# Optimization experiments

Hardware: AMD Instinct MI355X
Metric: run time of the kernel (lower is better)

## Reference

```python
import jax, jax.numpy as jnp
import numpy as np

B, CIN, COUT, K, STRIDE, PAD = 32, 64, 128, 3, 1, 1
IN_H, IN_W = 112, 112


def setup_inputs() -> dict:
    key = jax.random.key(0)
    k1, k2 = jax.random.split(key)
    # x_padded already has `PAD` rows/cols of zeros on each side, as in the torch module
    x = jax.random.normal(k1, (B, CIN, IN_H, IN_W), dtype=jnp.float32)
    x_padded = jnp.pad(x, ((0, 0), (0, 0), (PAD, PAD), (PAD, PAD)))
    weight = jax.random.normal(k2, (COUT, CIN, K, K), dtype=jnp.float32) * 0.1
    bias = jnp.zeros((COUT,), dtype=jnp.float32)
    return {
        "x_padded": x_padded,
        "in_height": IN_H,
        "in_width": IN_W,
        "weight": weight,
        "bias": bias,
    }


def reference(x_padded, in_height, in_width, weight, bias):
    # CustomConv2D.custom_conv2d: direct conv over the pre-padded input.
    # out[b,o,h,w] = sum_{i,kh,kw} x_padded[b,i,h*s+kh,w*s+kw] * weight[o,i,kh,kw] + bias[o]
    out = jax.lax.conv_general_dilated(
        x_padded, weight,
        window_strides=(STRIDE, STRIDE),
        padding="VALID",  # padding already applied to x_padded
        dimension_numbers=("NCHW", "OIHW", "NCHW"),
    )
    return out + bias[None, :, None, None]
```

## Files before the change

### kernel.cpp

```cpp
#include <hip/hip_runtime.h>

typedef __attribute__((ext_vector_type(8))) short short8;
typedef __attribute__((ext_vector_type(4))) float f32x4;
typedef __attribute__((ext_vector_type(4))) unsigned int u32x4;
typedef unsigned short u16;
typedef unsigned int u32;
typedef unsigned long long u64;

#define XH 114
#define XW 114
#define CINC 64
#define COUT 128
#define OH 112
#define OW 112
#define NB 32
#define KTOT 576

static __device__ __forceinline__ u16 f2bf(float f) {
    u32 x = __float_as_uint(f);
    u32 r = (x + 0x7fffu + ((x >> 16) & 1u)) >> 16;
    return (u16)r;
}

#define MFMA16(a, b, c) __builtin_amdgcn_mfma_f32_16x16x32_bf16((a), (b), (c), 0, 0, 0)

static __device__ __forceinline__ void gload16(const void* g, void* l) {
    __builtin_amdgcn_global_load_lds(
        (const __attribute__((address_space(1))) unsigned int*)g,
        (__attribute__((address_space(3))) unsigned int*)l, 16, 0, 0);
}


__global__ __launch_bounds__(256) void wcvt_reord(const float* __restrict__ w,
                                                  u16* __restrict__ wbf) {
    int i = blockIdx.x * 256 + threadIdx.x;
    int o = i / KTOT;
    int rem = i - o * KTOT;
    int khkw = rem >> 6;
    int ci = rem & 63;
    wbf[i] = f2bf(w[(o * CINC + ci) * 9 + khkw]);
}

__global__ __launch_bounds__(256) void xcvt(const float* __restrict__ x,
                                            u16* __restrict__ xb) {
    __shared__ u16 tile[XW * 70];
    const int blk = blockIdx.x;
    const int b = blk / XH;
    const int h = blk - b * XH;
    const int tid = threadIdx.x;

    #pragma unroll
    for (int it = 0; it < 15; ++it) {
        int idx = it * 256 + tid;
        if (idx < 32 * XW) {
            int cp = idx / XW;
            int w_ = idx - cp * XW;
            const float* s0 = x + ((size_t)(b * CINC + 2 * cp) * XH + h) * XW + w_;
            float a = s0[0];
            float c = s0[XH * XW];
            u32 pk = (u32)f2bf(a) | ((u32)f2bf(c) << 16);
            *(u32*)&tile[w_ * 70 + 2 * cp] = pk;
        }
    }
    __syncthreads();

    u16* dstrow = xb + (size_t)(b * XH + h) * (XW * CINC);
    #pragma unroll
    for (int p2 = 0; p2 < 4; ++p2) {
        int task = p2 * 256 + tid;
        if (task < XW * 8) {
            int w_ = task >> 3;
            int c8 = task & 7;
            const u32* s = (const u32*)&tile[w_ * 70 + c8 * 8];
            u32x4 v = {s[0], s[1], s[2], s[3]};
            int slot = c8 ^ ((2 * h + w_) & 7);
            *(u32x4*)(dstrow + w_ * CINC + slot * 8) = v;
        }
    }
}

__global__ __launch_bounds__(512, 4) void conv_r5(const u16* __restrict__ xb,
                                                  const u16* __restrict__ wbf,
                                                  const float* __restrict__ bias,
                                                  float* __restrict__ out) {
    __shared__ u16 ldsB[4 * XW * CINC];
    char* ldsc = (char*)ldsB;

    const int tid = threadIdx.x;
    int bid = blockIdx.x;
    {
        int xcd = bid & 7;
        bid = xcd * 224 + (bid >> 3);
    }
    const int b  = bid / 56;
    const int h0 = (bid - b * 56) * 2;

    const int lane = tid & 63;
    const int wv   = tid >> 6;

    {
        const char* src = (const char*)(xb + (size_t)(b * XH + h0) * (XW * CINC));
        #pragma unroll
        for (int it = 0; it < 8; ++it) {
            int off = it * 8192 + wv * 1024;
            if (off < 4 * XW * CINC * 2) {
                gload16(src + off + lane * 16, ldsc + off);
            }
        }
    }
    __syncthreads();

    const int l16  = lane & 15;
    const int lhi  = lane >> 4;
    const int wm   = wv & 3;
    const int wn   = wv >> 2;

    const u16* wrow0 = wbf + (wm * 32 + l16) * KTOT + lhi * 8;
    const u16* wrow1 = wrow0 + 16 * KTOT;

    f32x4 acc[2][7];
    const f32x4 zero = {0.f, 0.f, 0.f, 0.f};
    #pragma unroll
    for (int i = 0; i < 2; ++i)
        #pragma unroll
        for (int j = 0; j < 7; ++j) acc[i][j] = zero;

    short8 aA0 = *(const short8*)(wrow0);
    short8 aA1 = *(const short8*)(wrow1);
    short8 aB0, aB1;

    #pragma unroll 1
    for (int tt = 0; tt < 9; ++tt) {
        const int t0 = 2 * tt;
        aB0 = *(const short8*)(wrow0 + (t0 + 1) * 32);
        aB1 = *(const short8*)(wrow1 + (t0 + 1) * 32);

        const int kh = tt / 3;
        const int kw = tt - kh * 3;
        const int r  = wn + kh;
        const int pix0 = r * XW + kw + l16;
        const int hash = (2 * (h0 + r) + kw + l16) & 7;
        const int baddr0 = (pix0 << 7) + ((lhi ^ hash) << 4);

        {
            __builtin_amdgcn_s_setprio(1);
            #pragma unroll
            for (int nf = 0; nf < 7; ++nf) {
                short8 bf = *(const short8*)(ldsc + baddr0 + nf * 2048);
                acc[0][nf] = MFMA16(aA0, bf, acc[0][nf]);
                acc[1][nf] = MFMA16(aA1, bf, acc[1][nf]);
            }
            __builtin_amdgcn_s_setprio(0);
        }
        if (tt < 8) {
            aA0 = *(const short8*)(wrow0 + (t0 + 2) * 32);
            aA1 = *(const short8*)(wrow1 + (t0 + 2) * 32);
        }
        {
            __builtin_amdgcn_s_setprio(1);
            #pragma unroll
            for (int nf = 0; nf < 7; ++nf) {
                short8 bf = *(const short8*)(ldsc + (baddr0 ^ 0x40) + nf * 2048);
                acc[0][nf] = MFMA16(aB0, bf, acc[0][nf]);
                acc[1][nf] = MFMA16(aB1, bf, acc[1][nf]);
            }
            __builtin_amdgcn_s_setprio(0);
        }
    }

    float* outb = out + (size_t)b * COUT * (OH * OW) + (h0 + wn) * OW;
    #pragma unroll
    for (int mf = 0; mf < 2; ++mf) {
        #pragma unroll
        for (int j = 0; j < 4; ++j) {
            const int o = wm * 32 + mf * 16 + lhi * 4 + j;
            const float bv = bias[o];
            #pragma unroll
            for (int nf = 0; nf < 7; ++nf) {
                outb[(size_t)o * (OH * OW) + nf * 16 + l16] = acc[mf][nf][j] + bv;
            }
        }
    }
}


#define BK 32
#define NSTEP 18
#define LDB 40

__global__ __launch_bounds__(256) void wcvt_ident(const float* __restrict__ w,
                                                  u16* __restrict__ wbf) {
    int i = blockIdx.x * 256 + threadIdx.x;
    if (i < COUT * KTOT) wbf[i] = f2bf(w[i]);
}

__global__ __launch_bounds__(256) void conv_fb(const float* __restrict__ x,
                                               const u16* __restrict__ wbf,
                                               const float* __restrict__ bias,
                                               float* __restrict__ out) {
    __shared__ u16 ldsB[OW * LDB];
    const int tid = threadIdx.x;
    int bid = blockIdx.x;
    { int xcd = bid & 7; bid = xcd * 448 + (bid >> 3); }
    const int b = bid / OH;
    const int h = bid - b * OH;
    const float* xbp = x + (size_t)b * (CINC * XH * XW);
    float* outb = out + (size_t)b * (COUT * OH * OW) + h * OW;
    const int lane = tid & 63, wv = tid >> 6, l16 = lane & 15, lhi = lane >> 4;
    const int m0 = wv * 32;
    const int sk = tid >> 3, sn0 = (tid & 7) * 14;
    f32x4 acc[2][7];
    const f32x4 zero = {0.f, 0.f, 0.f, 0.f};
    #pragma unroll
    for (int i = 0; i < 2; ++i)
        #pragma unroll
        for (int j = 0; j < 7; ++j) acc[i][j] = zero;
    for (int t = 0; t < NSTEP; ++t) {
        const int kg = t * BK + sk;
        const int ci = kg / 9;
        const int r9 = kg - ci * 9;
        const int kh = r9 / 3, kw = r9 - (r9 / 3) * 3;
        const float* src = xbp + ((size_t)ci * XH + (h + kh)) * XW + kw + sn0;
        __syncthreads();
        #pragma unroll
        for (int i = 0; i < 14; ++i) ldsB[(sn0 + i) * LDB + sk] = f2bf(src[i]);
        __syncthreads();
        short8 afrag[2];
        #pragma unroll
        for (int mf = 0; mf < 2; ++mf)
            afrag[mf] = *(const short8*)(wbf + (m0 + mf * 16 + l16) * KTOT + t * BK + lhi * 8);
        #pragma unroll
        for (int nf = 0; nf < 7; ++nf) {
            short8 bfrag = *(const short8*)&ldsB[(nf * 16 + l16) * LDB + lhi * 8];
            acc[0][nf] = MFMA16(afrag[0], bfrag, acc[0][nf]);
            acc[1][nf] = MFMA16(afrag[1], bfrag, acc[1][nf]);
        }
    }
    #pragma unroll
    for (int mf = 0; mf < 2; ++mf)
        #pragma unroll
        for (int j = 0; j < 4; ++j) {
            const int o = m0 + mf * 16 + lhi * 4 + j;
            const float bv = bias[o];
            #pragma unroll
            for (int nf = 0; nf < 7; ++nf)
                outb[(size_t)o * (OH * OW) + nf * 16 + l16] = acc[mf][nf][j] + bv;
        }
}

extern "C" void kernel_launch(void* const* d_in, const int* in_sizes, int n_in,
                              void* d_out, int out_size, void* d_ws, size_t ws_size,
                              hipStream_t stream) {
    const float* x    = (const float*)d_in[0];
    const float* w    = (const float*)d_in[3];
    const float* bias = (const float*)d_in[4];
    float* out = (float*)d_out;

    const size_t WBYTES = (size_t)COUT * KTOT * 2;
    const size_t XBYTES = (size_t)NB * XH * XW * CINC * 2;
    if (ws_size >= WBYTES + XBYTES) {
        u16* wbf = (u16*)d_ws;
        u16* xb  = (u16*)((char*)d_ws + WBYTES);
        wcvt_reord<<<(COUT * KTOT) / 256, 256, 0, stream>>>(w, wbf);
        xcvt<<<NB * XH, 256, 0, stream>>>(x, xb);
        conv_r5<<<NB * 56, 512, 0, stream>>>(xb, wbf, bias, out);
    } else {
        u16* wbf = (u16*)d_ws;
        wcvt_ident<<<(COUT * KTOT + 255) / 256, 256, 0, stream>>>(w, wbf);
        conv_fb<<<NB * OH, 256, 0, stream>>>(x, wbf, bias, out);
    }
}
```

Baseline: 129.7 us.

## Make conv kernel persistent with double-buffered LDS tiles and register-resident weights

Result: faster. 122.1 us (-5.9%).

```diff
diff --git a/kernel.cpp b/kernel.cpp
--- a/kernel.cpp
+++ b/kernel.cpp
@@ -15,6 +15,7 @@
 #define OW 112
 #define NB 32
 #define KTOT 576
+#define TILEB 58368
 
 static __device__ __forceinline__ u16 f2bf(float f) {
     u32 x = __float_as_uint(f);
@@ -79,105 +80,108 @@
     }
 }
 
-__global__ __launch_bounds__(512, 4) void conv_r5(const u16* __restrict__ xb,
-                                                  const u16* __restrict__ wbf,
-                                                  const float* __restrict__ bias,
-                                                  float* __restrict__ out) {
-    __shared__ u16 ldsB[4 * XW * CINC];
-    char* ldsc = (char*)ldsB;
-
-    const int tid = threadIdx.x;
-    int bid = blockIdx.x;
-    {
-        int xcd = bid & 7;
-        bid = xcd * 224 + (bid >> 3);
-    }
-    const int b  = bid / 56;
-    const int h0 = (bid - b * 56) * 2;
-
+__global__ __launch_bounds__(512, 2) void conv_pers(const u16* __restrict__ xb,
+                                                    const u16* __restrict__ wbf,
+                                                    const float* __restrict__ bias,
+                                                    float* __restrict__ out) {
+    __shared__ u16 lds[2 * 4 * XW * CINC];
+    char* ldsc = (char*)lds;
+
+    const int tid  = threadIdx.x;
     const int lane = tid & 63;
     const int wv   = tid >> 6;
-
-    {
-        const char* src = (const char*)(xb + (size_t)(b * XH + h0) * (XW * CINC));
-        #pragma unroll
-        for (int it = 0; it < 8; ++it) {
-            int off = it * 8192 + wv * 1024;
-            if (off < 4 * XW * CINC * 2) {
-                gload16(src + off + lane * 16, ldsc + off);
-            }
-        }
-    }
-    __syncthreads();
-
     const int l16  = lane & 15;
     const int lhi  = lane >> 4;
     const int wm   = wv & 3;
     const int wn   = wv >> 2;
 
+    const int t0g = blockIdx.x * 7;
+
     const u16* wrow0 = wbf + (wm * 32 + l16) * KTOT + lhi * 8;
     const u16* wrow1 = wrow0 + 16 * KTOT;
-
-    f32x4 acc[2][7];
+    short8 areg[18][2];
+    #pragma unroll
+    for (int t = 0; t < 18; ++t) {
+        areg[t][0] = *(const short8*)(wrow0 + t * 32);
+        areg[t][1] = *(const short8*)(wrow1 + t * 32);
+    }
+
+    {
+        const char* src = (const char*)(xb + (size_t)((t0g / 56) * XH + (t0g % 56) * 2) * (XW * CINC));
+        #pragma unroll
+        for (int it = 0; it < 8; ++it) {
+            int off = it * 8192 + wv * 1024;
+            if (off < TILEB) gload16(src + off + lane * 16, ldsc + off);
+        }
+    }
+
     const f32x4 zero = {0.f, 0.f, 0.f, 0.f};
-    #pragma unroll
-    for (int i = 0; i < 2; ++i)
-        #pragma unroll
-        for (int j = 0; j < 7; ++j) acc[i][j] = zero;
-
-    short8 aA0 = *(const short8*)(wrow0);
-    short8 aA1 = *(const short8*)(wrow1);
-    short8 aB0, aB1;
 
     #pragma unroll 1
-    for (int tt = 0; tt < 9; ++tt) {
-        const int t0 = 2 * tt;
-        aB0 = *(const short8*)(wrow0 + (t0 + 1) * 32);
-        aB1 = *(const short8*)(wrow1 + (t0 + 1) * 32);
-
-        const int kh = tt / 3;
-        const int kw = tt - kh * 3;
-        const int r  = wn + kh;
-        const int pix0 = r * XW + kw + l16;
-        const int hash = (2 * (h0 + r) + kw + l16) & 7;
-        const int baddr0 = (pix0 << 7) + ((lhi ^ hash) << 4);
-
-        {
+    for (int i = 0; i < 7; ++i) {
+        __syncthreads();
+
+        if (i < 6) {
+            const int tg = t0g + i + 1;
+            const char* src = (const char*)(xb + (size_t)((tg / 56) * XH + (tg % 56) * 2) * (XW * CINC));
+            char* dstb = ldsc + ((i + 1) & 1) * TILEB;
+            #pragma unroll
+            for (int it = 0; it < 8; ++it) {
+                int off = it * 8192 + wv * 1024;
+                if (off < TILEB) gload16(src + off + lane * 16, dstb + off);
+            }
+        }
+
+        const int tg = t0g + i;
+        const int b  = tg / 56;
+        const int h0 = (tg - b * 56) * 2;
+        char* buf = ldsc + (i & 1) * TILEB;
+
+        f32x4 acc[2][7];
+        #pragma unroll
+        for (int mf = 0; mf < 2; ++mf)
+            #pragma unroll
+            for (int nf = 0; nf < 7; ++nf) acc[mf][nf] = zero;
+
+        #pragma unroll
+        for (int tt = 0; tt < 9; ++tt) {
+            const int kh = tt / 3;
+            const int kw = tt - kh * 3;
+            const int r  = wn + kh;
+            const int pix0 = r * XW + kw + l16;
+            const int hash = (2 * (h0 + r) + kw + l16) & 7;
+            const int ba0 = (pix0 << 7) + ((lhi ^ hash) << 4);
+
             __builtin_amdgcn_s_setprio(1);
             #pragma unroll
             for (int nf = 0; nf < 7; ++nf) {
-                short8 bf = *(const short8*)(ldsc + baddr0 + nf * 2048);
-                acc[0][nf] = MFMA16(aA0, bf, acc[0][nf]);
-                acc[1][nf] = MFMA16(aA1, bf, acc[1][nf]);
+                short8 bf = *(const short8*)(buf + ba0 + nf * 2048);
+                acc[0][nf] = MFMA16(areg[2 * tt][0], bf, acc[0][nf]);
+                acc[1][nf] = MFMA16(areg[2 * tt][1], bf, acc[1][nf]);
             }
             __builtin_amdgcn_s_setprio(0);
-        }
-        if (tt < 8) {
-            aA0 = *(const short8*)(wrow0 + (t0 + 2) * 32);
-            aA1 = *(const short8*)(wrow1 + (t0 + 2) * 32);
-        }
-        {
+
             __builtin_amdgcn_s_setprio(1);
             #pragma unroll
             for (int nf = 0; nf < 7; ++nf) {
-                short8 bf = *(const short8*)(ldsc + (baddr0 ^ 0x40) + nf * 2048);
-                acc[0][nf] = MFMA16(aB0, bf, acc[0][nf]);
-                acc[1][nf] = MFMA16(aB1, bf, acc[1][nf]);
+                short8 bf = *(const short8*)(buf + (ba0 ^ 0x40) + nf * 2048);
+                acc[0][nf] = MFMA16(areg[2 * tt + 1][0], bf, acc[0][nf]);
+                acc[1][nf] = MFMA16(areg[2 * tt + 1][1], bf, acc[1][nf]);
             }
             __builtin_amdgcn_s_setprio(0);
         }
-    }
-
-    float* outb = out + (size_t)b * COUT * (OH * OW) + (h0 + wn) * OW;
-    #pragma unroll
-    for (int mf = 0; mf < 2; ++mf) {
-        #pragma unroll
-        for (int j = 0; j < 4; ++j) {
-            const int o = wm * 32 + mf * 16 + lhi * 4 + j;
-            const float bv = bias[o];
-            #pragma unroll
-            for (int nf = 0; nf < 7; ++nf) {
-                outb[(size_t)o * (OH * OW) + nf * 16 + l16] = acc[mf][nf][j] + bv;
+
+        float* outb = out + (size_t)b * COUT * (OH * OW) + (h0 + wn) * OW;
+        #pragma unroll
+        for (int mf = 0; mf < 2; ++mf) {
+            #pragma unroll
+            for (int j = 0; j < 4; ++j) {
+                const int o = wm * 32 + mf * 16 + lhi * 4 + j;
+                const float bv = bias[o];
+                #pragma unroll
+                for (int nf = 0; nf < 7; ++nf) {
+                    outb[(size_t)o * (OH * OW) + nf * 16 + l16] = acc[mf][nf][j] + bv;
+                }
             }
         }
     }
@@ -263,7 +267,7 @@
         u16* xb  = (u16*)((char*)d_ws + WBYTES);
         wcvt_reord<<<(COUT * KTOT) / 256, 256, 0, stream>>>(w, wbf);
         xcvt<<<NB * XH, 256, 0, stream>>>(x, xb);
-        conv_r5<<<NB * 56, 512, 0, stream>>>(xb, wbf, bias, out);
+        conv_pers<<<256, 512, 0, stream>>>(xb, wbf, bias, out);
     } else {
         u16* wbf = (u16*)d_ws;
         wcvt_ident<<<(COUT * KTOT + 255) / 256, 256, 0, stream>>>(w, wbf);
```
